# Kernel optimization log

Measured on AMD Instinct MI355X. Metric: run time of the kernel, lower is better.

The kernel has to match this reference:

```python
import jax, jax.numpy as jnp
import numpy as np

RANK = 64          # rank
ENT_COMPS = 5      # ent_comps (1 time + 4 space components per rank slot)
REL_COMPS = 4      # rel_comps (quaternion / boost velocity)
N_ENT = 80000
N_REL = 500
B = 2000
INIT_SIZE = 0.001
SCALE = 1.0 / np.sqrt(RANK)
EPS = 1e-9


def _quat_mul(q, p):
    # Hamilton product of quaternions q, p: [..., 4] each, layout (w, x, y, z)
    qw, qx, qy, qz = q[..., 0], q[..., 1], q[..., 2], q[..., 3]
    pw, px, py, pz = p[..., 0], p[..., 1], p[..., 2], p[..., 3]
    return jnp.stack([
        qw * pw - qx * px - qy * py - qz * pz,
        qw * px + qx * pw + qy * pz - qz * py,
        qw * py - qx * pz + qy * pw + qz * px,
        qw * pz + qx * py - qy * px + qz * pw,
    ], axis=-1)


def lorentz_rotate(x, r):
    # x: [B, R, 5] Lorentz vectors (t, s4); r: [B, R, 4] rotation quaternion.
    # Spatial 4D isoclinic rotation via unit-quaternion left multiplication; time fixed.
    q = r * jax.lax.rsqrt(jnp.sum(r * r, axis=-1, keepdims=True) + EPS)
    t, s = x[..., :1], x[..., 1:]
    return jnp.concatenate([t, _quat_mul(q, s)], axis=-1)


def lorentz_boost(x, v):
    # x: [B, R, 5]; v: [B, R, 4] boost velocity (|v| < 1).
    t, s = x[..., :1], x[..., 1:]
    vn2 = jnp.clip(jnp.sum(v * v, axis=-1, keepdims=True), 0.0, 0.999)  # [B,R,1]
    gamma = jax.lax.rsqrt(1.0 - vn2)
    vs = jnp.sum(v * s, axis=-1, keepdims=True)
    t2 = gamma * (t + vs)
    s2 = s + (gamma * t + (gamma - 1.0) * vs / (vn2 + EPS)) * v
    return jnp.concatenate([t2, s2], axis=-1)


def setup_inputs() -> dict:
    key = jax.random.key(0)
    k = jax.random.split(key, 6)
    queries = jax.random.randint(k[0], (B, 3), 0, N_REL, dtype=jnp.int32)
    stru_entities = jax.random.normal(k[1], (N_ENT, 2 * RANK, ENT_COMPS), jnp.float32) * INIT_SIZE
    stru_rel_rotate = jax.random.normal(k[2], (N_REL, RANK, REL_COMPS), jnp.float32) * INIT_SIZE
    stru_rel_boosts = jax.random.normal(k[3], (N_REL, RANK, REL_COMPS), jnp.float32) * INIT_SIZE
    stru_atten = jax.random.normal(k[4], (N_REL, 1, ENT_COMPS * RANK), jnp.float32) * INIT_SIZE
    stru_rel_aux = jax.random.normal(k[5], (N_REL, 2, ENT_COMPS * RANK), jnp.float32) * INIT_SIZE
    return {
        "queries": queries,
        "stru_entities": stru_entities,
        "stru_rel_rotate": stru_rel_rotate,
        "stru_rel_boosts": stru_rel_boosts,
        "stru_atten": stru_atten,
        "stru_rel_aux": stru_rel_aux,
    }


def reference(queries, stru_entities, stru_rel_rotate, stru_rel_boosts, stru_atten, stru_rel_aux):
    b = queries.shape[0]
    D = ENT_COMPS * RANK  # 320
    h, r, t = queries[:, 0], queries[:, 1], queries[:, 2]

    slhs = stru_entities[h]                       # [B, 2R, 5]
    srhs = stru_entities[t]                       # [B, 2R, 5]
    lhs_re = slhs[:, :RANK]                       # [B, R, 5]
    lhs_im = slhs[:, RANK:].reshape(b, D)         # [B, D]
    rhs_re = srhs[:, :RANK].reshape(b, D)
    rhs_im = srhs[:, RANK:].reshape(b, D)

    rrot = stru_rel_rotate[r]                     # [B, R, 4]
    rboost = stru_rel_boosts[r]                   # [B, R, 4]
    atten = stru_atten[r]                         # [B, 1, D]
    aux = stru_rel_aux[r]                         # [B, 2, D]
    aux0, aux1 = aux[:, 0], aux[:, 1]

    to_re = stru_entities[:, :RANK].reshape(N_ENT, D)
    to_im = stru_entities[:, RANK:].reshape(N_ENT, D)

    rot = lorentz_rotate(lhs_re, rrot).reshape(b, D, 1)
    boo = lorentz_boost(lhs_re, rboost).reshape(b, D, 1)
    cands = jnp.concatenate([rot, boo], axis=-1)              # [B, D, 2]
    weights = jax.nn.softmax(jnp.matmul(atten * SCALE, cands), axis=-1)  # [B, 1, 2]
    lhs = jnp.sum(cands * weights, axis=-1)                   # [B, D]

    scores = (lhs * aux0 - lhs_im * aux1) @ to_re.T \
           + (lhs * aux1 + lhs_im * aux0) @ to_im.T           # [B, N_ENT]

    reg0 = jnp.sqrt(lhs_re.reshape(b, D) ** 2 + lhs_im ** 2)
    reg1 = jnp.sqrt(aux0 ** 2 + aux1 ** 2)
    reg2 = jnp.sqrt(rhs_re ** 2 + rhs_im ** 2) * (1.0 / 3.0)
    reg3 = jnp.sqrt(jnp.sum(rrot ** 2, axis=-1))
    reg4 = jnp.sqrt(jnp.sum(rboost ** 2, axis=-1))
    return scores, reg0, reg1, reg2, reg3, reg4
```

## Files before the change

### kernel.cpp

```cpp
#include <hip/hip_runtime.h>
#include <math.h>

#define RANK 64
#define D_DIM 320
#define K_DIM 640
#define N_ENT 80000
#define B_Q 2000
#define M_PAD 2048
#define NBLK_N 313
#define NT 10
#define SCALE_F 0.125f
#define EPS_F 1e-9f

#define OFF_SCORES 0ull
#define OFF_REG0 160000000ull
#define OFF_REG1 160640000ull
#define OFF_REG2 161280000ull
#define OFF_REG3 161920000ull
#define OFF_REG4 162048000ull

typedef __attribute__((ext_vector_type(8))) short short8v;
typedef __attribute__((ext_vector_type(4))) float floatx4;

typedef __attribute__((address_space(1))) const unsigned int gu32;
typedef __attribute__((address_space(3))) unsigned int lu32;

#define VMCNT6() asm volatile("s_waitcnt vmcnt(6)" ::: "memory")
#define VMCNT4() asm volatile("s_waitcnt vmcnt(4)" ::: "memory")
#define VMCNT0() asm volatile("s_waitcnt vmcnt(0)" ::: "memory")
#define LGKM0()  asm volatile("s_waitcnt lgkmcnt(0)" ::: "memory")

static __device__ __forceinline__ unsigned short f2bf(float f) {
    union { float f; unsigned int u; } a; a.f = f;
    unsigned int u = a.u;
    u += 0x7FFFu + ((u >> 16) & 1u);
    return (unsigned short)(u >> 16);
}

__global__ __launch_bounds__(64) void prep_kernel(
    const int* __restrict__ q,
    const float* __restrict__ ent,
    const float* __restrict__ rrot_t,
    const float* __restrict__ rboost_t,
    const float* __restrict__ atten_t,
    const float* __restrict__ aux_t,
    unsigned short* __restrict__ X,
    float* __restrict__ out)
{
    int b = blockIdx.x;
    int lane = threadIdx.x;
    unsigned short* Xrow = X + (size_t)b * K_DIM;

    if (b >= B_Q) {
        #pragma unroll
        for (int c = 0; c < 10; c++) Xrow[lane * 10 + c] = 0;
        return;
    }

    int h = q[3 * b + 0];
    int r = q[3 * b + 1];
    int t = q[3 * b + 2];

    const float* eh = ent + (size_t)h * K_DIM;
    const float* et = ent + (size_t)t * K_DIM;

    float4 rv = *(const float4*)(rrot_t + (size_t)r * 256 + lane * 4);
    float4 bv = *(const float4*)(rboost_t + (size_t)r * 256 + lane * 4);

    const float* xr = eh + lane * 5;
    float x0 = xr[0], x1 = xr[1], x2 = xr[2], x3 = xr[3], x4 = xr[4];

    float rr2 = rv.x * rv.x + rv.y * rv.y + rv.z * rv.z + rv.w * rv.w;
    float rb2 = bv.x * bv.x + bv.y * bv.y + bv.z * bv.z + bv.w * bv.w;

    float qinv = 1.0f / sqrtf(rr2 + EPS_F);
    float qw = rv.x * qinv, qx = rv.y * qinv, qy = rv.z * qinv, qz = rv.w * qinv;
    float pw = x1, px = x2, py = x3, pz = x4;
    float rot[5];
    rot[0] = x0;
    rot[1] = qw * pw - qx * px - qy * py - qz * pz;
    rot[2] = qw * px + qx * pw + qy * pz - qz * py;
    rot[3] = qw * py - qx * pz + qy * pw + qz * px;
    rot[4] = qw * pz + qx * py - qy * px + qz * pw;

    float vn2 = fminf(fmaxf(rb2, 0.0f), 0.999f);
    float sq = sqrtf(1.0f - vn2);
    float gamma = 1.0f / sq;
    float gm1 = vn2 / (sq * (1.0f + sq));
    float vs = bv.x * x1 + bv.y * x2 + bv.z * x3 + bv.w * x4;
    float boo[5];
    boo[0] = gamma * (x0 + vs);
    float coef = gamma * x0 + gm1 * vs / (vn2 + EPS_F);
    boo[1] = x1 + coef * bv.x;
    boo[2] = x2 + coef * bv.y;
    boo[3] = x3 + coef * bv.z;
    boo[4] = x4 + coef * bv.w;

    const float* at = atten_t + (size_t)r * D_DIM + lane * 5;
    float w0 = at[0] * rot[0] + at[1] * rot[1] + at[2] * rot[2] + at[3] * rot[3] + at[4] * rot[4];
    float w1 = at[0] * boo[0] + at[1] * boo[1] + at[2] * boo[2] + at[3] * boo[3] + at[4] * boo[4];
    #pragma unroll
    for (int off = 32; off; off >>= 1) {
        w0 += __shfl_xor(w0, off);
        w1 += __shfl_xor(w1, off);
    }
    w0 *= SCALE_F;
    w1 *= SCALE_F;
    float mx = fmaxf(w0, w1);
    float e0 = expf(w0 - mx), e1 = expf(w1 - mx);
    float inv = 1.0f / (e0 + e1);
    float wt0 = e0 * inv, wt1 = e1 * inv;

    const float* a0p = aux_t + (size_t)r * 640 + lane * 5;
    const float* a1p = a0p + D_DIM;
    float xre[5] = {x0, x1, x2, x3, x4};

    #pragma unroll
    for (int c = 0; c < 5; c++) {
        int d = lane * 5 + c;
        float lhs = wt0 * rot[c] + wt1 * boo[c];
        float im = eh[D_DIM + d];
        float a0 = a0p[c], a1 = a1p[c];
        Xrow[d]         = f2bf(lhs * a0 - im * a1);
        Xrow[D_DIM + d] = f2bf(lhs * a1 + im * a0);
        out[OFF_REG0 + (size_t)b * D_DIM + d] = sqrtf(xre[c] * xre[c] + im * im);
        out[OFF_REG1 + (size_t)b * D_DIM + d] = sqrtf(a0 * a0 + a1 * a1);
        float tre = et[d], tim = et[D_DIM + d];
        out[OFF_REG2 + (size_t)b * D_DIM + d] = sqrtf(tre * tre + tim * tim) * (1.0f / 3.0f);
    }
    out[OFF_REG3 + (size_t)b * RANK + lane] = sqrtf(rr2);
    out[OFF_REG4 + (size_t)b * RANK + lane] = sqrtf(rb2);
}

__global__ __launch_bounds__(256) void convE_kernel(
    const float* __restrict__ Ef, unsigned short* __restrict__ Eb)
{
    const size_t n4 = (size_t)N_ENT * K_DIM / 4;
    size_t stride = (size_t)gridDim.x * blockDim.x;
    for (size_t v = (size_t)blockIdx.x * blockDim.x + threadIdx.x; v < n4; v += stride) {
        float4 f = ((const float4*)Ef)[v];
        ushort4 u;
        u.x = f2bf(f.x); u.y = f2bf(f.y); u.z = f2bf(f.z); u.w = f2bf(f.w);
        ((ushort4*)Eb)[v] = u;
    }
}

__global__ __launch_bounds__(512, 1) void gemm256(
    const unsigned short* __restrict__ X,
    const unsigned short* __restrict__ Eb,
    float* __restrict__ C)
{
    __shared__ unsigned short lds[65536];

    const int tid = threadIdx.x;
    const int lane = tid & 63;
    const int wid = tid >> 6;
    const int wm = wid >> 2;
    const int wn = wid & 3;

    int bid = blockIdx.x;
    const int m0 = (bid & 7) * 256;
    const int n0 = (bid >> 3) * 256;

    const int fr = lane & 15;
    const int kq = lane >> 4;
    const int cbs8 = (kq ^ ((fr >> 1) & 3)) * 8;

    floatx4 acc[8][4];
    #pragma unroll
    for (int i = 0; i < 8; i++)
        #pragma unroll
        for (int j = 0; j < 4; j++) acc[i][j] = (floatx4)0.0f;

    const int srow = tid >> 2;
    const int scb = tid & 3;

    auto stage_ht = [&](int bufOff, int kt, int h) {
        const int mat = h & 1, kk = h >> 1;
        const int base = bufOff + mat * 16384 + kk * 8192;
        #pragma unroll
        for (int l = 0; l < 2; l++) {
            int row = srow + l * 128;
            int colg = kk * 32 + ((scb ^ ((row >> 1) & 3)) * 8);
            const unsigned short* gp;
            if (mat == 0) {
                gp = X + (size_t)(m0 + row) * K_DIM + kt * 64 + colg;
            } else {
                int grow = n0 + row;
                if (grow > N_ENT - 1) grow = N_ENT - 1;
                gp = Eb + (size_t)grow * K_DIM + kt * 64 + colg;
            }
            __builtin_amdgcn_global_load_lds((gu32*)gp,
                (lu32*)&lds[base + row * 32 + scb * 8], 16, 0, 0);
        }
    };

#define PHASE(KK, IH, WAITM, PF)                                              \
    {                                                                         \
        const unsigned short* Ab_ = lds + bufo + (KK) * 8192;                 \
        const unsigned short* Bb_ = lds + bufo + 16384 + (KK) * 8192;         \
        short8v a_[4], b_[4];                                                 \
        _Pragma("unroll")                                                     \
        for (int i2 = 0; i2 < 4; i2++) {                                      \
            int row = wm * 128 + ((IH) * 4 + i2) * 16 + fr;                   \
            a_[i2] = *(const short8v*)&Ab_[row * 32 + cbs8];                  \
        }                                                                     \
        _Pragma("unroll")                                                     \
        for (int j = 0; j < 4; j++) {                                         \
            int row = wn * 64 + j * 16 + fr;                                  \
            b_[j] = *(const short8v*)&Bb_[row * 32 + cbs8];                   \
        }                                                                     \
        if (PF) stage_ht(nbo, t + 1, (KK) * 2 + (IH));                        \
        WAITM();                                                              \
        __builtin_amdgcn_s_barrier();                                         \
        LGKM0();                                                              \
        __builtin_amdgcn_sched_barrier(0);                                    \
        __builtin_amdgcn_s_setprio(1);                                        \
        _Pragma("unroll")                                                     \
        for (int i2 = 0; i2 < 4; i2++)                                        \
            _Pragma("unroll")                                                 \
            for (int j = 0; j < 4; j++)                                       \
                acc[(IH) * 4 + i2][j] = __builtin_amdgcn_mfma_f32_16x16x32_bf16( \
                    a_[i2], b_[j], acc[(IH) * 4 + i2][j], 0, 0, 0);           \
        __builtin_amdgcn_s_setprio(0);                                        \
        __builtin_amdgcn_s_barrier();                                        \
    }

    #pragma unroll
    for (int h = 0; h < 4; h++) stage_ht(0, 0, h);
    VMCNT0();
    __builtin_amdgcn_s_barrier();

    for (int t = 0; t < NT - 1; t++) {
        const int bufo = (t & 1) * 32768;
        const int nbo = bufo ^ 32768;
        PHASE(0, 0, VMCNT6, true)
        PHASE(0, 1, VMCNT4, true)
        PHASE(1, 0, VMCNT6, true)
        PHASE(1, 1, VMCNT4, true)
    }
    {
        const int t = NT - 1;
        const int bufo = (t & 1) * 32768;
        const int nbo = bufo ^ 32768;
        (void)nbo;
        PHASE(0, 0, VMCNT4, false)
        PHASE(0, 1, VMCNT0, false)
        PHASE(1, 0, VMCNT0, false)
        PHASE(1, 1, VMCNT0, false)
    }
#undef PHASE

    const int rb = kq * 4;
    #pragma unroll
    for (int i = 0; i < 8; i++) {
        #pragma unroll
        for (int j = 0; j < 4; j++) {
            int row = m0 + wm * 128 + i * 16 + rb;
            int col = n0 + wn * 64 + j * 16 + fr;
            if (col < N_ENT) {
                #pragma unroll
                for (int r = 0; r < 4; r++) {
                    if (row + r < B_Q)
                        C[(size_t)(row + r) * N_ENT + col] = acc[i][j][r];
                }
            }
        }
    }
}

__global__ __launch_bounds__(256) void gemm_mfma_fb(
    const unsigned short* __restrict__ X,
    const float* __restrict__ Ef,
    float* __restrict__ C)
{
    __shared__ unsigned short As[128 * 32];
    __shared__ unsigned short Bs[128 * 32];

    const int tid = threadIdx.x;
    const int lane = tid & 63;
    const int wave = tid >> 6;
    const int wm = wave >> 1, wn = wave & 1;
    const int m0 = blockIdx.x * 128;
    const int n0 = blockIdx.y * 128;

    floatx4 acc[4][4];
    #pragma unroll
    for (int i = 0; i < 4; i++)
        #pragma unroll
        for (int j = 0; j < 4; j++) acc[i][j] = (floatx4)0.0f;

    const int srow = tid >> 2;
    const int scol = (tid & 3) * 8;
    const int fr = lane & 15;
    const int kb = (lane >> 4) * 8;
    const int brow_f = tid >> 1;
    const int bcol_f = (tid & 1) * 16;

    for (int k0 = 0; k0 < K_DIM; k0 += 32) {
        __syncthreads();
        #pragma unroll
        for (int r = 0; r < 2; r++) {
            const unsigned short* gp = X + (size_t)(m0 + srow + r * 64) * K_DIM + k0 + scol;
            __builtin_amdgcn_global_load_lds((gu32*)gp, (lu32*)(As + (size_t)(r * 64 + srow) * 32 + scol), 16, 0, 0);
        }
        {
            const float* ep = Ef + (size_t)(n0 + brow_f) * K_DIM + k0 + bcol_f;
            float4 f0 = *(const float4*)(ep);
            float4 f1 = *(const float4*)(ep + 4);
            float4 f2 = *(const float4*)(ep + 8);
            float4 f3 = *(const float4*)(ep + 12);
            short8v p0, p1;
            p0[0] = (short)f2bf(f0.x); p0[1] = (short)f2bf(f0.y);
            p0[2] = (short)f2bf(f0.z); p0[3] = (short)f2bf(f0.w);
            p0[4] = (short)f2bf(f1.x); p0[5] = (short)f2bf(f1.y);
            p0[6] = (short)f2bf(f1.z); p0[7] = (short)f2bf(f1.w);
            p1[0] = (short)f2bf(f2.x); p1[1] = (short)f2bf(f2.y);
            p1[2] = (short)f2bf(f2.z); p1[3] = (short)f2bf(f2.w);
            p1[4] = (short)f2bf(f3.x); p1[5] = (short)f2bf(f3.y);
            p1[6] = (short)f2bf(f3.z); p1[7] = (short)f2bf(f3.w);
            *(short8v*)(Bs + (size_t)brow_f * 32 + bcol_f) = p0;
            *(short8v*)(Bs + (size_t)brow_f * 32 + bcol_f + 8) = p1;
        }
        __syncthreads();

        short8v a[4], b[4];
        #pragma unroll
        for (int i = 0; i < 4; i++)
            a[i] = *(const short8v*)(As + (size_t)(wm * 64 + i * 16 + fr) * 32 + kb);
        #pragma unroll
        for (int j = 0; j < 4; j++)
            b[j] = *(const short8v*)(Bs + (size_t)(wn * 64 + j * 16 + fr) * 32 + kb);

        #pragma unroll
        for (int i = 0; i < 4; i++)
            #pragma unroll
            for (int j = 0; j < 4; j++)
                acc[i][j] = __builtin_amdgcn_mfma_f32_16x16x32_bf16(a[i], b[j], acc[i][j], 0, 0, 0);
    }

    const int rbase = (lane >> 4) * 4;
    #pragma unroll
    for (int i = 0; i < 4; i++) {
        #pragma unroll
        for (int j = 0; j < 4; j++) {
            int row = m0 + wm * 64 + i * 16 + rbase;
            int col = n0 + wn * 64 + j * 16 + fr;
            #pragma unroll
            for (int r = 0; r < 4; r++) {
                if (row + r < B_Q)
                    C[(size_t)(row + r) * N_ENT + col] = acc[i][j][r];
            }
        }
    }
}

extern "C" void kernel_launch(void* const* d_in, const int* in_sizes, int n_in,
                              void* d_out, int out_size, void* d_ws, size_t ws_size,
                              hipStream_t stream) {
    const int* queries = (const int*)d_in[0];
    const float* ent = (const float*)d_in[1];
    const float* rrot = (const float*)d_in[2];
    const float* rboost = (const float*)d_in[3];
    const float* atten = (const float*)d_in[4];
    const float* aux = (const float*)d_in[5];
    float* out = (float*)d_out;

    unsigned short* X = (unsigned short*)d_ws;
    const size_t offE = (size_t)M_PAD * K_DIM * 2;
    const size_t needE = (size_t)N_ENT * K_DIM * 2;
    unsigned short* Eb = (unsigned short*)((char*)d_ws + offE);
    bool pre = (ws_size >= offE + needE);

    prep_kernel<<<M_PAD, 64, 0, stream>>>(queries, ent, rrot, rboost, atten, aux, X, out);

    if (pre) {
        convE_kernel<<<2048, 256, 0, stream>>>(ent, Eb);
        gemm256<<<8 * NBLK_N, 512, 0, stream>>>(X, Eb, out + OFF_SCORES);
    } else {
        dim3 grid(M_PAD / 128, N_ENT / 128);
        gemm_mfma_fb<<<grid, 256, 0, stream>>>(X, ent, out + OFF_SCORES);
    }
}
```

Baseline: 403.5 us.

## Fuse prep and bf16 conversion kernels; merge GEMM phases into two per tile

```diff
diff --git a/kernel.cpp b/kernel.cpp
--- a/kernel.cpp
+++ b/kernel.cpp
@@ -25,7 +25,6 @@
 typedef __attribute__((address_space(1))) const unsigned int gu32;
 typedef __attribute__((address_space(3))) unsigned int lu32;
 
-#define VMCNT6() asm volatile("s_waitcnt vmcnt(6)" ::: "memory")
 #define VMCNT4() asm volatile("s_waitcnt vmcnt(4)" ::: "memory")
 #define VMCNT0() asm volatile("s_waitcnt vmcnt(0)" ::: "memory")
 #define LGKM0()  asm volatile("s_waitcnt lgkmcnt(0)" ::: "memory")
@@ -37,7 +36,8 @@
     return (unsigned short)(u >> 16);
 }
 
-__global__ __launch_bounds__(64) void prep_kernel(
+static __device__ __forceinline__ void prep_row(
+    int b, int lane,
     const int* __restrict__ q,
     const float* __restrict__ ent,
     const float* __restrict__ rrot_t,
@@ -47,8 +47,6 @@
     unsigned short* __restrict__ X,
     float* __restrict__ out)
 {
-    int b = blockIdx.x;
-    int lane = threadIdx.x;
     unsigned short* Xrow = X + (size_t)b * K_DIM;
 
     if (b >= B_Q) {
@@ -132,17 +130,41 @@
     out[OFF_REG4 + (size_t)b * RANK + lane] = sqrtf(rb2);
 }
 
-__global__ __launch_bounds__(256) void convE_kernel(
-    const float* __restrict__ Ef, unsigned short* __restrict__ Eb)
+#define PREP_BLKS 512
+#define CONV_BLKS 2048
+__global__ __launch_bounds__(256) void prepconv_kernel(
+    const int* __restrict__ q,
+    const float* __restrict__ ent,
+    const float* __restrict__ rrot_t,
+    const float* __restrict__ rboost_t,
+    const float* __restrict__ atten_t,
+    const float* __restrict__ aux_t,
+    unsigned short* __restrict__ X,
+    unsigned short* __restrict__ Eb,
+    float* __restrict__ out)
 {
-    const size_t n4 = (size_t)N_ENT * K_DIM / 4;
-    size_t stride = (size_t)gridDim.x * blockDim.x;
-    for (size_t v = (size_t)blockIdx.x * blockDim.x + threadIdx.x; v < n4; v += stride) {
-        float4 f = ((const float4*)Ef)[v];
-        ushort4 u;
-        u.x = f2bf(f.x); u.y = f2bf(f.y); u.z = f2bf(f.z); u.w = f2bf(f.w);
-        ((ushort4*)Eb)[v] = u;
-    }
+    if (blockIdx.x < PREP_BLKS) {
+        int b = blockIdx.x * 4 + (threadIdx.x >> 6);
+        prep_row(b, threadIdx.x & 63, q, ent, rrot_t, rboost_t, atten_t, aux_t, X, out);
+    } else {
+        const size_t n4 = (size_t)N_ENT * K_DIM / 4;
+        size_t stride = (size_t)CONV_BLKS * 256;
+        for (size_t v = (size_t)(blockIdx.x - PREP_BLKS) * 256 + threadIdx.x; v < n4; v += stride) {
+            float4 f = ((const float4*)ent)[v];
+            ushort4 u;
+            u.x = f2bf(f.x); u.y = f2bf(f.y); u.z = f2bf(f.z); u.w = f2bf(f.w);
+            ((ushort4*)Eb)[v] = u;
+        }
+    }
+}
+
+__global__ __launch_bounds__(64) void prep_kernel(
+    const int* __restrict__ q, const float* __restrict__ ent,
+    const float* __restrict__ rrot_t, const float* __restrict__ rboost_t,
+    const float* __restrict__ atten_t, const float* __restrict__ aux_t,
+    unsigned short* __restrict__ X, float* __restrict__ out)
+{
+    prep_row(blockIdx.x, threadIdx.x, q, ent, rrot_t, rboost_t, atten_t, aux_t, X, out);
 }
 
 __global__ __launch_bounds__(512, 1) void gemm256(
@@ -195,14 +217,14 @@
         }
     };
 
-#define PHASE(KK, IH, WAITM, PF)                                              \
+#define PHASE2(KK, WAITM, PF)                                                 \
     {                                                                         \
         const unsigned short* Ab_ = lds + bufo + (KK) * 8192;                 \
         const unsigned short* Bb_ = lds + bufo + 16384 + (KK) * 8192;         \
-        short8v a_[4], b_[4];                                                 \
+        short8v a_[8], b_[4];                                                 \
         _Pragma("unroll")                                                     \
-        for (int i2 = 0; i2 < 4; i2++) {                                      \
-            int row = wm * 128 + ((IH) * 4 + i2) * 16 + fr;                   \
+        for (int i2 = 0; i2 < 8; i2++) {                                      \
+            int row = wm * 128 + i2 * 16 + fr;                                \
             a_[i2] = *(const short8v*)&Ab_[row * 32 + cbs8];                  \
         }                                                                     \
         _Pragma("unroll")                                                     \
@@ -210,20 +232,23 @@
             int row = wn * 64 + j * 16 + fr;                                  \
             b_[j] = *(const short8v*)&Bb_[row * 32 + cbs8];                   \
         }                                                                     \
-        if (PF) stage_ht(nbo, t + 1, (KK) * 2 + (IH));                        \
+        if (PF) {                                                             \
+            stage_ht(nbo, t + 1, (KK) * 2 + 0);                               \
+            stage_ht(nbo, t + 1, (KK) * 2 + 1);                               \
+        }                                                                     \
         WAITM();                                                              \
         __builtin_amdgcn_s_barrier();                                         \
         LGKM0();                                                              \
         __builtin_amdgcn_sched_barrier(0);                                    \
         __builtin_amdgcn_s_setprio(1);                                        \
         _Pragma("unroll")                                                     \
-        for (int i2 = 0; i2 < 4; i2++)                                        \
+        for (int i2 = 0; i2 < 8; i2++)                                        \
             _Pragma("unroll")                                                 \
             for (int j = 0; j < 4; j++)                                       \
-                acc[(IH) * 4 + i2][j] = __builtin_amdgcn_mfma_f32_16x16x32_bf16( \
-                    a_[i2], b_[j], acc[(IH) * 4 + i2][j], 0, 0, 0);           \
+                acc[i2][j] = __builtin_amdgcn_mfma_f32_16x16x32_bf16(         \
+                    a_[i2], b_[j], acc[i2][j], 0, 0, 0);                      \
         __builtin_amdgcn_s_setprio(0);                                        \
-        __builtin_amdgcn_s_barrier();                                        \
+        __builtin_amdgcn_s_barrier();                                         \
     }
 
     #pragma unroll
@@ -234,22 +259,18 @@
     for (int t = 0; t < NT - 1; t++) {
         const int bufo = (t & 1) * 32768;
         const int nbo = bufo ^ 32768;
-        PHASE(0, 0, VMCNT6, true)
-        PHASE(0, 1, VMCNT4, true)
-        PHASE(1, 0, VMCNT6, true)
-        PHASE(1, 1, VMCNT4, true)
+        PHASE2(0, VMCNT4, true)
+        PHASE2(1, VMCNT4, true)
     }
     {
         const int t = NT - 1;
         const int bufo = (t & 1) * 32768;
         const int nbo = bufo ^ 32768;
         (void)nbo;
-        PHASE(0, 0, VMCNT4, false)
-        PHASE(0, 1, VMCNT0, false)
-        PHASE(1, 0, VMCNT0, false)
-        PHASE(1, 1, VMCNT0, false)
-    }
-#undef PHASE
+        PHASE2(0, VMCNT0, false)
+        PHASE2(1, VMCNT0, false)
+    }
+#undef PHASE2
 
     const int rb = kq * 4;
     #pragma unroll
@@ -372,12 +393,12 @@
     unsigned short* Eb = (unsigned short*)((char*)d_ws + offE);
     bool pre = (ws_size >= offE + needE);
 
-    prep_kernel<<<M_PAD, 64, 0, stream>>>(queries, ent, rrot, rboost, atten, aux, X, out);
-
     if (pre) {
-        convE_kernel<<<2048, 256, 0, stream>>>(ent, Eb);
+        prepconv_kernel<<<PREP_BLKS + CONV_BLKS, 256, 0, stream>>>(
+            queries, ent, rrot, rboost, atten, aux, X, Eb, out);
         gemm256<<<8 * NBLK_N, 512, 0, stream>>>(X, Eb, out + OFF_SCORES);
     } else {
+        prep_kernel<<<M_PAD, 64, 0, stream>>>(queries, ent, rrot, rboost, atten, aux, X, out);
         dim3 grid(M_PAD / 128, N_ENT / 128);
         gemm_mfma_fb<<<grid, 256, 0, stream>>>(X, ent, out + OFF_SCORES);
     }
```

Result: no change. 411.0 us (+1.8%).
